# Kernel tuning notes

Measured on AMD Instinct MI355X. Metric: run time of the kernel, lower is better.

Reference implementation:

```python
import jax, jax.numpy as jnp
from jax import lax
import numpy as np

RADIUS = 4
SIGMA_I = 10.0
SIGMA_X = 4.0
NUM_CLASSES = 6
PAD = RADIUS - 1          # ConstantPad3d(radius-1)
WIN = 2 * PAD + 1         # 7: window width per spatial axis
EPS = 2.220446049250313e-16  # np.finfo(float).eps used as pad value


def _dist_and_offsets():
    # Spatial Gaussian dist[x,y,z] = exp(-(x^2+y^2+z^2)/sigmaX^2) inside ball of radius RADIUS, else 0
    coords = np.arange(-PAD, PAD + 1)
    xx, yy, zz = np.meshgrid(coords, coords, coords, indexing='ij')
    d2 = xx ** 2 + yy ** 2 + zz ** 2
    dist = np.where(d2 < RADIUS ** 2, np.exp(-d2 / SIGMA_X ** 2), 0.0).astype(np.float32).ravel()
    idx = np.arange(WIN)
    ox, oy, oz = np.meshgrid(idx, idx, idx, indexing='ij')
    offs = np.stack([ox, oy, oz], axis=-1).reshape(-1, 3).astype(np.int32)  # (343, 3)
    return jnp.asarray(offs), jnp.asarray(dist)


def _soft_ncut(batch, preds):
    # batch: (B,1,D,H,W) intensities; preds: (B,K,D,H,W) soft class assignments
    B, C, D, H, W = batch.shape
    K = preds.shape[1]
    pw = ((0, 0), (0, 0), (PAD, PAD), (PAD, PAD), (PAD, PAD))
    pb = jnp.pad(batch, pw, constant_values=EPS)
    pp = jnp.pad(preds, pw, constant_values=EPS)
    offs, dist = _dist_and_offsets()

    def step(carry, xs):
        aA, aV = carry
        off, dv = xs
        # bilateral weight for this window offset: exp(-(I_p - I_{p+off})^2 / sigmaI^2) * dist(off)
        sb = lax.dynamic_slice(pb, (0, 0, off[0], off[1], off[2]), (B, C, D, H, W))
        w = jnp.exp(-jnp.square(batch - sb) / (SIGMA_I ** 2)) * dv        # (B,1,D,H,W)
        sp = lax.dynamic_slice(pp, (0, 0, off[0], off[1], off[2]), (B, K, D, H, W))
        # assocA contribution: sum_p preds * (w * shifted_preds); assocV: sum_p preds * w
        aA = aA + jnp.einsum('bcdhw,bkdhw,bkdhw->bk', w, sp, preds)
        aV = aV + jnp.einsum('bcdhw,bkdhw->bk', w, preds)
        return (aA, aV), None

    init = (jnp.zeros((B, K), jnp.float32), jnp.zeros((B, K), jnp.float32))
    (assocA, assocV), _ = lax.scan(jax.checkpoint(step), init, (offs, dist))
    assoc = jnp.sum(assocA / assocV, axis=-1)                              # (B,)
    return jnp.float32(NUM_CLASSES) - assoc


def setup_inputs() -> dict:
    key = jax.random.key(0)
    kb, kp = jax.random.split(key)
    batch = jax.random.uniform(kb, (8, 1, 32, 32, 32), dtype=jnp.float32)
    preds = jax.random.uniform(kp, (8, 6, 32, 32, 32), dtype=jnp.float32)
    return {"batch": batch, "preds": preds}


def reference(batch, preds):
    return _soft_ncut(batch, preds)
```

## Files before the change

kernel.cpp:

```cpp
#include <hip/hip_runtime.h>

#define EPSV 2.220446049250313e-16f
#define C3F  (-0.09016844005555896f)
#define SSCL 0.1201122408786449f
#define EPSS (EPSV * SSCL)

typedef float f2 __attribute__((ext_vector_type(2)));
typedef float f4 __attribute__((ext_vector_type(4)));


__global__ __launch_bounds__(256) void ncut_main(const float* __restrict__ batch,
                                                 const float* __restrict__ preds,
                                                 float* __restrict__ wsA,
                                                 float* __restrict__ wsV) {
    constexpr int LS = 38;
    constexpr int PLANE = 38 * LS;
    __shared__ float sAll[7 * PLANE];
    __shared__ float redBuf[4][12];

    const int tid = threadIdx.x;
    const int bx  = blockIdx.x;
    const int oz  = bx >> 8;
    const int b   = (bx >> 5) & 7;
    const int d   = bx & 31;

    const int z   = d + oz;
    const bool zok = (z < 32);

    {
        f4* a4 = (f4*)sAll;
        const f4 bpad = {EPSS, EPSS, EPSS, EPSS};
        const f4 ppad = {EPSV, EPSV, EPSV, EPSV};
        for (int i = tid; i < 2527; i += 256) a4[i] = (i < 361) ? bpad : ppad;
    }
    __syncthreads();

    const int hh = tid >> 3;
    const int j4 = (tid & 7) << 2;
    if (zok) {
        const float* bsrc = batch + ((size_t)b * 32 + z) * 1024 + hh * 32 + j4;
        const float* psrc = preds + ((size_t)b * 6 * 32 + z) * 1024 + hh * 32 + j4;
        {
            f4 v = *(const f4*)bsrc;
            v *= SSCL;
            float* dst = sAll + (hh + 3) * LS + (j4 + 3);
            dst[0] = v.x; dst[1] = v.y; dst[2] = v.z; dst[3] = v.w;
        }
        #pragma unroll
        for (int p = 0; p < 6; ++p) {
            f4 v = *(const f4*)(psrc + (size_t)p * 32768);
            float* dst = sAll + (p + 1) * PLANE + (hh + 3) * LS + (j4 + 3);
            dst[0] = v.x; dst[1] = v.y; dst[2] = v.z; dst[3] = v.w;
        }
    }

    const int h  = hh;
    const int v0 = j4;
    f4 Ip = *(const f4*)&batch[((size_t)b * 32 + d) * 1024 + h * 32 + v0];
    Ip *= SSCL;

    __syncthreads();

    f4 wsum = {};
    f4 acc[6] = {};
    const int czz = oz * oz;
    const float gz = (float)czz * C3F;

    #pragma unroll
    for (int dy = 0; dy < 7; ++dy) {
        const int oy  = dy - 3;
        const int cyy = oy * oy;
        if (czz + cyy >= 16) continue;
        if (oz == 0 && oy < 0) continue;

        const int rowOff = (h + dy) * LS + v0;
        const f2* base = (const f2*)(sAll + rowOff);
        constexpr int PL2 = PLANE / 2;

        f2 tb0 = base[0], tb1 = base[1], tb2 = base[2], tb3 = base[3], tb4 = base[4];
        f2 c0 = base[PL2 + 0], c1 = base[PL2 + 1], c2 = base[PL2 + 2],
           c3 = base[PL2 + 3], c4 = base[PL2 + 4];

        float bseg[10] = {tb0.x, tb0.y, tb1.x, tb1.y, tb2.x, tb2.y, tb3.x, tb3.y, tb4.x, tb4.y};

        f4 wv[7] = {};
        #pragma unroll
        for (int dx = 0; dx < 7; ++dx) {
            const int ox  = dx - 3;
            const int cxx = ox * ox;
            if (czz + cyy + cxx < 16 && !(oz == 0 && oy == 0 && ox <= 0)) {
                const float g = gz + (float)(cyy + cxx) * C3F;
                f4 bv = {bseg[dx], bseg[dx + 1], bseg[dx + 2], bseg[dx + 3]};
                f4 dI = Ip - bv;
                f4 t  = (f4){g, g, g, g} - dI * dI;
                f4 w;
                w.x = __builtin_amdgcn_exp2f(t.x);
                w.y = __builtin_amdgcn_exp2f(t.y);
                w.z = __builtin_amdgcn_exp2f(t.z);
                w.w = __builtin_amdgcn_exp2f(t.w);
                wv[dx] = w;
                wsum += w;
            }
        }

        #pragma unroll
        for (int k = 0; k < 6; ++k) {
            f2 n0, n1, n2, n3, n4;
            if (k < 5) {
                const f2* nb = base + (size_t)(k + 2) * PL2;
                n0 = nb[0]; n1 = nb[1]; n2 = nb[2]; n3 = nb[3]; n4 = nb[4];
            }
            float pseg[10] = {c0.x, c0.y, c1.x, c1.y, c2.x, c2.y, c3.x, c3.y, c4.x, c4.y};
            f4 a = acc[k];
            #pragma unroll
            for (int dx = 0; dx < 7; ++dx) {
                const int ox  = dx - 3;
                const int cxx = ox * ox;
                if (czz + cyy + cxx < 16 && !(oz == 0 && oy == 0 && ox <= 0))
                    a += wv[dx] * (f4){pseg[dx], pseg[dx + 1], pseg[dx + 2], pseg[dx + 3]};
            }
            acc[k] = a;
            if (k < 5) { c0 = n0; c1 = n1; c2 = n2; c3 = n3; c4 = n4; }
        }
    }

    f4 S = {};
    if ((d < oz) || (h < 3) || (h > 28) || (v0 == 0) || (v0 == 28)) {
        const float edz = __builtin_amdgcn_exp2f(gz);
        #pragma unroll
        for (int oy = -3; oy <= 3; ++oy) {
            #pragma unroll
            for (int ox = -3; ox <= 3; ++ox) {
                const int d2c = oy * oy + ox * ox;
                if (czz + d2c >= 16) continue;
                if (oz == 0 && (oy < 0 || (oy == 0 && ox <= 0))) continue;
                const float dist = edz * __builtin_exp2f((float)d2c * C3F);
                const bool sc = (d < oz) || (h < oy) || (h > 31 + oy);
                #pragma unroll
                for (int j = 0; j < 4; ++j) {
                    const int xj = v0 + j;
                    bool m = sc;
                    if (ox > 0) m = m || (xj < ox);
                    if (ox < 0) m = m || (xj > 31 + ox);
                    S[j] += m ? dist : 0.0f;
                }
            }
        }
    }
    {
        f4 dIe = Ip - (f4){EPSS, EPSS, EPSS, EPSS};
        f4 e4;
        e4.x = __builtin_amdgcn_exp2f(-dIe.x * dIe.x);
        e4.y = __builtin_amdgcn_exp2f(-dIe.y * dIe.y);
        e4.z = __builtin_amdgcn_exp2f(-dIe.z * dIe.z);
        e4.w = __builtin_amdgcn_exp2f(-dIe.w * dIe.w);
        wsum += e4 * S;
    }

    float pA[6], pV[6];
    #pragma unroll
    for (int k = 0; k < 6; ++k) {
        const size_t pc = (((size_t)b * 6 + k) * 32 + d) * 1024 + h * 32 + v0;
        f4 pcv = *(const f4*)&preds[pc];
        float dA = acc[k].x * pcv.x + acc[k].y * pcv.y + acc[k].z * pcv.z + acc[k].w * pcv.w;
        float hA = acc[k].x + acc[k].y + acc[k].z + acc[k].w;
        float dV = wsum.x * pcv.x + wsum.y * pcv.y + wsum.z * pcv.z + wsum.w * pcv.w;
        pA[k] = 2.0f * dA;
        pV[k] = dV + hA;
        if (oz == 0) {
            pA[k] += pcv.x * pcv.x + pcv.y * pcv.y + pcv.z * pcv.z + pcv.w * pcv.w;
            pV[k] += pcv.x + pcv.y + pcv.z + pcv.w;
        }
    }

    #pragma unroll
    for (int k = 0; k < 6; ++k) {
        #pragma unroll
        for (int off = 32; off > 0; off >>= 1) {
            pA[k] += __shfl_down(pA[k], off);
            pV[k] += __shfl_down(pV[k], off);
        }
    }
    const int lane = tid & 63, wave = tid >> 6;
    if (lane == 0) {
        #pragma unroll
        for (int k = 0; k < 6; ++k) {
            redBuf[wave][k]     = pA[k];
            redBuf[wave][6 + k] = pV[k];
        }
    }
    __syncthreads();
    if (tid < 12) {
        float s = redBuf[0][tid] + redBuf[1][tid] + redBuf[2][tid] + redBuf[3][tid];
        if (tid < 6) wsA[bx * 6 + tid] = s;
        else         wsV[bx * 6 + (tid - 6)] = s;
    }
}

__global__ __launch_bounds__(128) void ncut_final(const float* __restrict__ wsA,
                                                  const float* __restrict__ wsV,
                                                  float* __restrict__ out) {
    __shared__ float redBuf[2][12];
    const int b = blockIdx.x;
    const int t = threadIdx.x;
    const int oz = t >> 5, dd = t & 31;
    const int bx = oz * 256 + b * 32 + dd;
    float a[6], v[6];
    #pragma unroll
    for (int k = 0; k < 6; ++k) {
        a[k] = wsA[(size_t)bx * 6 + k];
        v[k] = wsV[(size_t)bx * 6 + k];
    }
    #pragma unroll
    for (int k = 0; k < 6; ++k) {
        #pragma unroll
        for (int off = 32; off > 0; off >>= 1) {
            a[k] += __shfl_down(a[k], off);
            v[k] += __shfl_down(v[k], off);
        }
    }
    const int lane = t & 63, wave = t >> 6;
    if (lane == 0) {
        #pragma unroll
        for (int k = 0; k < 6; ++k) {
            redBuf[wave][k]     = a[k];
            redBuf[wave][6 + k] = v[k];
        }
    }
    __syncthreads();
    if (t == 0) {
        float s = 0.f;
        #pragma unroll
        for (int k = 0; k < 6; ++k) {
            float sa = redBuf[0][k] + redBuf[1][k];
            float sv = redBuf[0][6 + k] + redBuf[1][6 + k];
            s += sa / sv;
        }
        out[b] = 6.0f - s;
    }
}

extern "C" void kernel_launch(void* const* d_in, const int* in_sizes, int n_in,
                              void* d_out, int out_size, void* d_ws, size_t ws_size,
                              hipStream_t stream) {
    const float* batch = (const float*)d_in[0];
    const float* preds = (const float*)d_in[1];
    float* out = (float*)d_out;
    float* wsA = (float*)d_ws;
    float* wsV = wsA + 1024 * 6;

    ncut_main<<<1024, 256, 0, stream>>>(batch, preds, wsA, wsV);
    ncut_final<<<8, 128, 0, stream>>>(wsA, wsV, out);
}
```

Baseline: 30.56 us.

## Process two z-offsets per block sharing one staged source plane

Each block now stages a single source z-plane of batch and preds into shared memory and computes contributions for two z-offsets (pr and pr+2) against two different center planes, halving the grid to 512 blocks. Because the window is indexed by source plane, the padding loads of out-of-range z-planes go away, and the out-of-range z correction for oz=0 is handled by a closed-form sum. This cuts redundant LDS staging and global loads and balances the work per block. In exchange it raises register pressure from two accumulator sets and leaves fewer blocks to hide latency.

```diff
diff --git a/kernel.cpp b/kernel.cpp
--- a/kernel.cpp
+++ b/kernel.cpp
@@ -7,6 +7,15 @@
 
 typedef float f2 __attribute__((ext_vector_type(2)));
 typedef float f4 __attribute__((ext_vector_type(4)));
+
+__device__ __forceinline__ f4 exp4(f4 t) {
+    f4 w;
+    w.x = __builtin_amdgcn_exp2f(t.x);
+    w.y = __builtin_amdgcn_exp2f(t.y);
+    w.z = __builtin_amdgcn_exp2f(t.z);
+    w.w = __builtin_amdgcn_exp2f(t.w);
+    return w;
+}
 
 
 __global__ __launch_bounds__(256) void ncut_main(const float* __restrict__ batch,
@@ -15,17 +24,20 @@
                                                  float* __restrict__ wsV) {
     constexpr int LS = 38;
     constexpr int PLANE = 38 * LS;
+    constexpr int PL2 = PLANE / 2;
     __shared__ float sAll[7 * PLANE];
-    __shared__ float redBuf[4][12];
+    __shared__ float redBuf[4][24];
 
     const int tid = threadIdx.x;
     const int bx  = blockIdx.x;
-    const int oz  = bx >> 8;
-    const int b   = (bx >> 5) & 7;
-    const int d   = bx & 31;
-
-    const int z   = d + oz;
-    const bool zok = (z < 32);
+    const int b   = bx & 7;
+    const int z   = (bx >> 3) & 31;
+    const int pr  = bx >> 8;
+
+    const int oz0 = pr,     oz1 = pr + 2;
+    const int d0  = z - oz0, d1 = z - oz1;
+    const int czz0 = oz0 * oz0, czz1 = oz1 * oz1;
+    const int dl0 = d0 < 0 ? 0 : d0, dl1 = d1 < 0 ? 0 : d1;
 
     {
         f4* a4 = (f4*)sAll;
@@ -37,69 +49,64 @@
 
     const int hh = tid >> 3;
     const int j4 = (tid & 7) << 2;
-    if (zok) {
+    {
         const float* bsrc = batch + ((size_t)b * 32 + z) * 1024 + hh * 32 + j4;
         const float* psrc = preds + ((size_t)b * 6 * 32 + z) * 1024 + hh * 32 + j4;
-        {
-            f4 v = *(const f4*)bsrc;
-            v *= SSCL;
-            float* dst = sAll + (hh + 3) * LS + (j4 + 3);
-            dst[0] = v.x; dst[1] = v.y; dst[2] = v.z; dst[3] = v.w;
-        }
+        f4 v = *(const f4*)bsrc;
+        v *= SSCL;
+        float* dst = sAll + (hh + 3) * LS + (j4 + 3);
+        dst[0] = v.x; dst[1] = v.y; dst[2] = v.z; dst[3] = v.w;
         #pragma unroll
         for (int p = 0; p < 6; ++p) {
-            f4 v = *(const f4*)(psrc + (size_t)p * 32768);
-            float* dst = sAll + (p + 1) * PLANE + (hh + 3) * LS + (j4 + 3);
-            dst[0] = v.x; dst[1] = v.y; dst[2] = v.z; dst[3] = v.w;
-        }
-    }
-
-    const int h  = hh;
-    const int v0 = j4;
-    f4 Ip = *(const f4*)&batch[((size_t)b * 32 + d) * 1024 + h * 32 + v0];
-    Ip *= SSCL;
-
-    __syncthreads();
-
-    f4 wsum = {};
-    f4 acc[6] = {};
-    const int czz = oz * oz;
-    const float gz = (float)czz * C3F;
+            f4 w = *(const f4*)(psrc + (size_t)p * 32768);
+            float* dq = sAll + (p + 1) * PLANE + (hh + 3) * LS + (j4 + 3);
+            dq[0] = w.x; dq[1] = w.y; dq[2] = w.z; dq[3] = w.w;
+        }
+    }
+
+    const int h = hh, v0 = j4;
+    f4 Ip0 = *(const f4*)&batch[((size_t)b * 32 + dl0) * 1024 + h * 32 + v0];
+    f4 Ip1 = *(const f4*)&batch[((size_t)b * 32 + dl1) * 1024 + h * 32 + v0];
+    Ip0 *= SSCL; Ip1 *= SSCL;
+
+    __syncthreads();
+
+    f4 wsum0 = {}, wsum1 = {};
+    f4 acc0[6] = {}, acc1[6] = {};
 
     #pragma unroll
     for (int dy = 0; dy < 7; ++dy) {
-        const int oy  = dy - 3;
+        const int oy = dy - 3;
         const int cyy = oy * oy;
-        if (czz + cyy >= 16) continue;
-        if (oz == 0 && oy < 0) continue;
+        const bool act0 = (czz0 + cyy < 16) && !(oz0 == 0 && oy < 0);
+        const bool act1 = (czz1 + cyy < 16);
 
         const int rowOff = (h + dy) * LS + v0;
         const f2* base = (const f2*)(sAll + rowOff);
-        constexpr int PL2 = PLANE / 2;
 
         f2 tb0 = base[0], tb1 = base[1], tb2 = base[2], tb3 = base[3], tb4 = base[4];
-        f2 c0 = base[PL2 + 0], c1 = base[PL2 + 1], c2 = base[PL2 + 2],
-           c3 = base[PL2 + 3], c4 = base[PL2 + 4];
-
+        f2 p0 = base[PL2], p1 = base[PL2 + 1], p2 = base[PL2 + 2],
+           p3 = base[PL2 + 3], p4 = base[PL2 + 4];
         float bseg[10] = {tb0.x, tb0.y, tb1.x, tb1.y, tb2.x, tb2.y, tb3.x, tb3.y, tb4.x, tb4.y};
 
-        f4 wv[7] = {};
+        f4 wv0[7] = {}, wv1[7] = {};
         #pragma unroll
         for (int dx = 0; dx < 7; ++dx) {
-            const int ox  = dx - 3;
+            const int ox = dx - 3;
             const int cxx = ox * ox;
-            if (czz + cyy + cxx < 16 && !(oz == 0 && oy == 0 && ox <= 0)) {
-                const float g = gz + (float)(cyy + cxx) * C3F;
-                f4 bv = {bseg[dx], bseg[dx + 1], bseg[dx + 2], bseg[dx + 3]};
-                f4 dI = Ip - bv;
-                f4 t  = (f4){g, g, g, g} - dI * dI;
-                f4 w;
-                w.x = __builtin_amdgcn_exp2f(t.x);
-                w.y = __builtin_amdgcn_exp2f(t.y);
-                w.z = __builtin_amdgcn_exp2f(t.z);
-                w.w = __builtin_amdgcn_exp2f(t.w);
-                wv[dx] = w;
-                wsum += w;
+            const int cyx = cyy + cxx;
+            f4 bv = {bseg[dx], bseg[dx + 1], bseg[dx + 2], bseg[dx + 3]};
+            if (act0 && (czz0 + cyx < 16) && !(oz0 == 0 && oy == 0 && ox <= 0)) {
+                const float g = (float)(czz0 + cyx) * C3F;
+                f4 dI = Ip0 - bv;
+                f4 w = exp4((f4){g, g, g, g} - dI * dI);
+                wv0[dx] = w; wsum0 += w;
+            }
+            if (act1 && (czz1 + cyx < 16)) {
+                const float g = (float)(czz1 + cyx) * C3F;
+                f4 dI = Ip1 - bv;
+                f4 w = exp4((f4){g, g, g, g} - dI * dI);
+                wv1[dx] = w; wsum1 += w;
             }
         }
 
@@ -110,90 +117,127 @@
                 const f2* nb = base + (size_t)(k + 2) * PL2;
                 n0 = nb[0]; n1 = nb[1]; n2 = nb[2]; n3 = nb[3]; n4 = nb[4];
             }
-            float pseg[10] = {c0.x, c0.y, c1.x, c1.y, c2.x, c2.y, c3.x, c3.y, c4.x, c4.y};
-            f4 a = acc[k];
-            #pragma unroll
-            for (int dx = 0; dx < 7; ++dx) {
-                const int ox  = dx - 3;
-                const int cxx = ox * ox;
-                if (czz + cyy + cxx < 16 && !(oz == 0 && oy == 0 && ox <= 0))
-                    a += wv[dx] * (f4){pseg[dx], pseg[dx + 1], pseg[dx + 2], pseg[dx + 3]};
-            }
-            acc[k] = a;
-            if (k < 5) { c0 = n0; c1 = n1; c2 = n2; c3 = n3; c4 = n4; }
-        }
-    }
-
-    f4 S = {};
-    if ((d < oz) || (h < 3) || (h > 28) || (v0 == 0) || (v0 == 28)) {
-        const float edz = __builtin_amdgcn_exp2f(gz);
-        #pragma unroll
-        for (int oy = -3; oy <= 3; ++oy) {
-            #pragma unroll
-            for (int ox = -3; ox <= 3; ++ox) {
-                const int d2c = oy * oy + ox * ox;
-                if (czz + d2c >= 16) continue;
-                if (oz == 0 && (oy < 0 || (oy == 0 && ox <= 0))) continue;
-                const float dist = edz * __builtin_exp2f((float)d2c * C3F);
-                const bool sc = (d < oz) || (h < oy) || (h > 31 + oy);
+            float pseg[10] = {p0.x, p0.y, p1.x, p1.y, p2.x, p2.y, p3.x, p3.y, p4.x, p4.y};
+            if (act0) {
+                f4 a = acc0[k];
                 #pragma unroll
-                for (int j = 0; j < 4; ++j) {
-                    const int xj = v0 + j;
-                    bool m = sc;
-                    if (ox > 0) m = m || (xj < ox);
-                    if (ox < 0) m = m || (xj > 31 + ox);
-                    S[j] += m ? dist : 0.0f;
+                for (int dx = 0; dx < 7; ++dx)
+                    a += wv0[dx] * (f4){pseg[dx], pseg[dx + 1], pseg[dx + 2], pseg[dx + 3]};
+                acc0[k] = a;
+            }
+            if (act1) {
+                f4 a = acc1[k];
+                #pragma unroll
+                for (int dx = 0; dx < 7; ++dx)
+                    a += wv1[dx] * (f4){pseg[dx], pseg[dx + 1], pseg[dx + 2], pseg[dx + 3]};
+                acc1[k] = a;
+            }
+            if (k < 5) { p0 = n0; p1 = n1; p2 = n2; p3 = n3; p4 = n4; }
+        }
+    }
+
+    float pA[2][6], pV[2][6];
+    #pragma unroll
+    for (int c = 0; c < 2; ++c) {
+        const int ozc = c ? oz1 : oz0;
+        const int dcv = c ? d1 : d0;
+        const int dlc = c ? dl1 : dl0;
+        const int czz = ozc * ozc;
+        f4 Ip   = c ? Ip1 : Ip0;
+        f4 wsum = c ? wsum1 : wsum0;
+        f4* acc = c ? acc1 : acc0;
+
+        f4 S = {};
+        if ((dcv < ozc) || (h < 3) || (h > 28) || (v0 == 0) || (v0 == 28)) {
+            const float edz = __builtin_amdgcn_exp2f((float)czz * C3F);
+            #pragma unroll
+            for (int oy = -3; oy <= 3; ++oy) {
+                #pragma unroll
+                for (int ox = -3; ox <= 3; ++ox) {
+                    const int d2c = oy * oy + ox * ox;
+                    if (czz + d2c >= 16) continue;
+                    if (ozc == 0 && (oy < 0 || (oy == 0 && ox <= 0))) continue;
+                    const float dist = edz * __builtin_exp2f((float)d2c * C3F);
+                    const bool sc = (dcv < ozc) || (h < oy) || (h > 31 + oy);
+                    #pragma unroll
+                    for (int j = 0; j < 4; ++j) {
+                        const int xj = v0 + j;
+                        bool m = sc;
+                        if (ox > 0) m = m || (xj < ox);
+                        if (ox < 0) m = m || (xj > 31 + ox);
+                        S[j] += m ? dist : 0.0f;
+                    }
                 }
             }
         }
-    }
-    {
+        if (ozc == 0) {
+            float Sz = 0.f;
+            #pragma unroll
+            for (int ozp = 1; ozp <= 3; ++ozp) {
+                if (dcv + ozp >= 32) {
+                    #pragma unroll
+                    for (int oy = -3; oy <= 3; ++oy) {
+                        #pragma unroll
+                        for (int ox = -3; ox <= 3; ++ox) {
+                            const int d2 = ozp * ozp + oy * oy + ox * ox;
+                            if (d2 < 16) Sz += __builtin_exp2f((float)d2 * C3F);
+                        }
+                    }
+                }
+            }
+            S += (f4){Sz, Sz, Sz, Sz};
+        }
         f4 dIe = Ip - (f4){EPSS, EPSS, EPSS, EPSS};
-        f4 e4;
-        e4.x = __builtin_amdgcn_exp2f(-dIe.x * dIe.x);
-        e4.y = __builtin_amdgcn_exp2f(-dIe.y * dIe.y);
-        e4.z = __builtin_amdgcn_exp2f(-dIe.z * dIe.z);
-        e4.w = __builtin_amdgcn_exp2f(-dIe.w * dIe.w);
-        wsum += e4 * S;
-    }
-
-    float pA[6], pV[6];
-    #pragma unroll
-    for (int k = 0; k < 6; ++k) {
-        const size_t pc = (((size_t)b * 6 + k) * 32 + d) * 1024 + h * 32 + v0;
-        f4 pcv = *(const f4*)&preds[pc];
-        float dA = acc[k].x * pcv.x + acc[k].y * pcv.y + acc[k].z * pcv.z + acc[k].w * pcv.w;
-        float hA = acc[k].x + acc[k].y + acc[k].z + acc[k].w;
-        float dV = wsum.x * pcv.x + wsum.y * pcv.y + wsum.z * pcv.z + wsum.w * pcv.w;
-        pA[k] = 2.0f * dA;
-        pV[k] = dV + hA;
-        if (oz == 0) {
-            pA[k] += pcv.x * pcv.x + pcv.y * pcv.y + pcv.z * pcv.z + pcv.w * pcv.w;
-            pV[k] += pcv.x + pcv.y + pcv.z + pcv.w;
-        }
-    }
-
-    #pragma unroll
-    for (int k = 0; k < 6; ++k) {
-        #pragma unroll
-        for (int off = 32; off > 0; off >>= 1) {
-            pA[k] += __shfl_down(pA[k], off);
-            pV[k] += __shfl_down(pV[k], off);
-        }
-    }
+        f4 e4v = exp4(-(dIe * dIe));
+        wsum += e4v * S;
+
+        #pragma unroll
+        for (int k = 0; k < 6; ++k) {
+            const size_t pc = (((size_t)b * 6 + k) * 32 + dlc) * 1024 + h * 32 + v0;
+            f4 pcv = *(const f4*)&preds[pc];
+            float dA = acc[k].x * pcv.x + acc[k].y * pcv.y + acc[k].z * pcv.z + acc[k].w * pcv.w;
+            float hA = acc[k].x + acc[k].y + acc[k].z + acc[k].w;
+            float dV = wsum.x * pcv.x + wsum.y * pcv.y + wsum.z * pcv.z + wsum.w * pcv.w;
+            pA[c][k] = 2.0f * dA;
+            pV[c][k] = dV + hA;
+            if (ozc == 0) {
+                pA[c][k] += pcv.x * pcv.x + pcv.y * pcv.y + pcv.z * pcv.z + pcv.w * pcv.w;
+                pV[c][k] += pcv.x + pcv.y + pcv.z + pcv.w;
+            }
+        }
+    }
+
+    #pragma unroll
+    for (int c = 0; c < 2; ++c)
+        #pragma unroll
+        for (int k = 0; k < 6; ++k) {
+            #pragma unroll
+            for (int off = 32; off > 0; off >>= 1) {
+                pA[c][k] += __shfl_down(pA[c][k], off);
+                pV[c][k] += __shfl_down(pV[c][k], off);
+            }
+        }
     const int lane = tid & 63, wave = tid >> 6;
     if (lane == 0) {
         #pragma unroll
-        for (int k = 0; k < 6; ++k) {
-            redBuf[wave][k]     = pA[k];
-            redBuf[wave][6 + k] = pV[k];
-        }
-    }
-    __syncthreads();
-    if (tid < 12) {
-        float s = redBuf[0][tid] + redBuf[1][tid] + redBuf[2][tid] + redBuf[3][tid];
-        if (tid < 6) wsA[bx * 6 + tid] = s;
-        else         wsV[bx * 6 + (tid - 6)] = s;
+        for (int c = 0; c < 2; ++c)
+            #pragma unroll
+            for (int k = 0; k < 6; ++k) {
+                redBuf[wave][c * 12 + k]     = pA[c][k];
+                redBuf[wave][c * 12 + 6 + k] = pV[c][k];
+            }
+    }
+    __syncthreads();
+    if (tid < 24) {
+        const int c = tid / 12, r = tid % 12;
+        const int dcv = c ? d1 : d0;
+        const int ozc = c ? oz1 : oz0;
+        if (dcv >= 0) {
+            float s = redBuf[0][tid] + redBuf[1][tid] + redBuf[2][tid] + redBuf[3][tid];
+            const size_t task = ((size_t)b * 32 + dcv) * 4 + ozc;
+            if (r < 6) wsA[task * 6 + r] = s;
+            else       wsV[task * 6 + (r - 6)] = s;
+        }
     }
 }
 
@@ -203,13 +247,14 @@
     __shared__ float redBuf[2][12];
     const int b = blockIdx.x;
     const int t = threadIdx.x;
-    const int oz = t >> 5, dd = t & 31;
-    const int bx = oz * 256 + b * 32 + dd;
+    const int d = t >> 2, oz = t & 3;
+    const bool valid = (d + oz <= 31);
+    const size_t task = ((size_t)b * 32 + d) * 4 + oz;
     float a[6], v[6];
     #pragma unroll
     for (int k = 0; k < 6; ++k) {
-        a[k] = wsA[(size_t)bx * 6 + k];
-        v[k] = wsV[(size_t)bx * 6 + k];
+        a[k] = valid ? wsA[task * 6 + k] : 0.0f;
+        v[k] = valid ? wsV[task * 6 + k] : 0.0f;
     }
     #pragma unroll
     for (int k = 0; k < 6; ++k) {
@@ -249,6 +294,6 @@
     float* wsA = (float*)d_ws;
     float* wsV = wsA + 1024 * 6;
 
-    ncut_main<<<1024, 256, 0, stream>>>(batch, preds, wsA, wsV);
+    ncut_main<<<512, 256, 0, stream>>>(batch, preds, wsA, wsV);
     ncut_final<<<8, 128, 0, stream>>>(wsA, wsV, out);
 }
```

Result: slower. 31.45 us (+2.9%).
